# Performance work log

Hardware: AMD Instinct MI355X
Metric: run time of the kernel (lower is better)

## Reference

```python
import jax, jax.numpy as jnp
import numpy as np

DIM = 128
CODEBOOK_SIZE = 1024


def setup_inputs() -> dict:
    key = jax.random.key(0)
    kx, ke = jax.random.split(key)
    x = jax.random.normal(kx, (16, 4096, DIM), dtype=jnp.float32)
    # kaiming_uniform_ on (codebook_size, dim): bound = sqrt(6 / fan_in), fan_in = dim
    bound = float(np.sqrt(6.0 / DIM))
    embed = jax.random.uniform(ke, (CODEBOOK_SIZE, DIM), dtype=jnp.float32,
                               minval=-bound, maxval=bound)
    return {"x": x, "embed": embed}


def reference(x, embed):
    orig_shape = x.shape
    flat = x.reshape(-1, x.shape[-1])                     # [N, D]
    x2 = jnp.sum(flat * flat, axis=1, keepdims=True)      # [N, 1]
    e2 = jnp.sum(embed * embed, axis=1)                   # [K]
    dist = -(x2 - 2.0 * (flat @ embed.T) + e2[None, :])   # [N, K]
    embed_ind = jnp.argmax(dist, axis=-1)                 # [N]
    embed_ind = embed_ind.reshape(orig_shape[:-1])        # [B, S]
    quantize = jnp.take(embed, embed_ind, axis=0)         # [B, S, D]
    return quantize, embed_ind
```

## Files before the change

### kernel.cpp

```cpp
#include <hip/hip_runtime.h>

#define DIM     128
#define NCODES  1024
#define TILE_M  64
#define BSTR    272
#define FLAGThr 0.018f
#define RPB     4
#define RGRID   1024

typedef __attribute__((ext_vector_type(8))) _Float16 half8;
typedef __attribute__((ext_vector_type(4))) _Float16 half4;
typedef __attribute__((ext_vector_type(4))) float    f32x4;


__global__ __launch_bounds__(256) void setup_kernel(
    const float* __restrict__ embed, double* __restrict__ e2d,
    float* __restrict__ e2f, _Float16* __restrict__ eh,
    float* __restrict__ embedT, int* __restrict__ cnt)
{
  __shared__ float tile[64][132];
  __shared__ double psum[4][64];
  if (blockIdx.x == 0 && threadIdx.x == 0) *cnt = 0;
  const int c0 = blockIdx.x * 64;
  const int t  = threadIdx.x;

  const f32x4* E4 = (const f32x4*)(embed + (size_t)c0 * DIM);
  #pragma unroll
  for (int i = 0; i < 8; ++i) {
    int e = t + i * 256;
    int r = e >> 5, c4 = e & 31;
    f32x4 v = E4[e];
    *(f32x4*)&tile[r][c4 * 4] = v;
    half4 h;
    h[0] = (_Float16)v[0]; h[1] = (_Float16)v[1];
    h[2] = (_Float16)v[2]; h[3] = (_Float16)v[3];
    *(half4*)&eh[(size_t)(c0 + r) * DIM + c4 * 4] = h;
  }
  __syncthreads();

  {
    int r = t & 63, part = t >> 6;
    double s = 0.0;
    #pragma unroll
    for (int k = 0; k < 32; ++k) {
      float v = tile[r][part * 32 + k];
      s += (double)v * v;
    }
    psum[part][r] = s;
  }
  __syncthreads();
  if (t < 64) {
    double s = psum[0][t] + psum[1][t] + psum[2][t] + psum[3][t];
    e2d[c0 + t] = s;
    e2f[c0 + t] = (float)s;
  }

  #pragma unroll
  for (int i = 0; i < 32; ++i) {
    int idx = t + i * 256;
    int k = idx >> 6, c = idx & 63;
    embedT[(size_t)k * NCODES + c0 + c] = tile[c][k];
  }
}

__global__ __launch_bounds__(256, 2) void pass1_kernel(
    const float* __restrict__ x, const float* __restrict__ embed,
    const _Float16* __restrict__ eh, const float* __restrict__ e2f,
    float* __restrict__ outQ, float* __restrict__ outIdx,
    int* __restrict__ cnt, int* __restrict__ list)
{
  __shared__ __align__(16) unsigned char lds[256 * BSTR];
  __shared__ float rb_best[4][TILE_M];
  __shared__ float rb_sec [4][TILE_M];
  __shared__ int   fidx[TILE_M];

  const int tid  = threadIdx.x;
  const int row0 = blockIdx.x * TILE_M;
  _Float16* xh = (_Float16*)lds;

  {
    const f32x4* x4 = (const f32x4*)(x + (size_t)row0 * DIM);
    #pragma unroll
    for (int i = 0; i < 8; ++i) {
      int e = tid + i * 256;
      int r = e >> 5, c4 = e & 31;
      f32x4 v = x4[e];
      half4 h;
      h[0] = (_Float16)v[0]; h[1] = (_Float16)v[1];
      h[2] = (_Float16)v[2]; h[3] = (_Float16)v[3];
      *(half4*)&xh[r * 136 + c4 * 4] = h;
    }
  }
  __syncthreads();

  const int l  = tid & 63, w = tid >> 6;
  const int rl = l & 15,  q = l >> 4;
  const int col0 = q * 8;

  half8 afrag[4][4];
  #pragma unroll
  for (int m = 0; m < 4; ++m)
    #pragma unroll
    for (int ks = 0; ks < 4; ++ks)
      afrag[m][ks] = *(const half8*)&xh[(m * 16 + rl) * 136 + ks * 32 + col0];

  float bestp[16], secp[16];
  #pragma unroll
  for (int s = 0; s < 16; ++s) { bestp[s] = -3.0e38f; secp[s] = -3.3e38f; }

  f32x4 t0[16];
  {
    const f32x4* src = (const f32x4*)eh;
    #pragma unroll
    for (int i = 0; i < 16; ++i) t0[i] = src[tid + i * 256];
  }
  __syncthreads();

  #pragma unroll
  for (int st = 0; st < 4; ++st) {
    #pragma unroll
    for (int i = 0; i < 16; ++i) {
      int e = tid + i * 256;
      *(f32x4*)&lds[(e >> 4) * BSTR + (e & 15) * 16] = t0[i];
    }
    f32x4 t1[16];
    if (st < 3) {
      const f32x4* src = (const f32x4*)(eh + (size_t)(st + 1) * 256 * DIM);
      #pragma unroll
      for (int i = 0; i < 16; ++i) t1[i] = src[tid + i * 256];
    }
    float vinit[4];
    #pragma unroll
    for (int sub = 0; sub < 4; ++sub)
      vinit[sub] = fmaf(-0.5f, e2f[st * 256 + w * 64 + sub * 16 + rl], -16.0f);

    __syncthreads();

    #pragma unroll
    for (int sub = 0; sub < 4; ++sub) {
      const int codeL  = w * 64 + sub * 16 + rl;
      const int mycode = st * 256 + codeL;
      half8 bfrag[4];
      #pragma unroll
      for (int ks = 0; ks < 4; ++ks)
        bfrag[ks] = *(const half8*)&lds[codeL * BSTR + ks * 64 + q * 16];
      f32x4 acc[4];
      #pragma unroll
      for (int m = 0; m < 4; ++m)
        acc[m] = (f32x4){vinit[sub], vinit[sub], vinit[sub], vinit[sub]};
      #pragma unroll
      for (int ks = 0; ks < 4; ++ks)
        #pragma unroll
        for (int m = 0; m < 4; ++m)
          acc[m] = __builtin_amdgcn_mfma_f32_16x16x32_f16(afrag[m][ks], bfrag[ks], acc[m], 0, 0, 0);
      #pragma unroll
      for (int m = 0; m < 4; ++m)
        #pragma unroll
        for (int r = 0; r < 4; ++r) {
          const int s = m * 4 + r;
          float scp = __int_as_float((__float_as_int(acc[m][r]) & ~1023) | mycode);
          secp[s]  = __builtin_amdgcn_fmed3f(scp, bestp[s], secp[s]);
          bestp[s] = fmaxf(bestp[s], scp);
        }
    }
    if (st < 3) {
      __syncthreads();
      #pragma unroll
      for (int i = 0; i < 16; ++i) t0[i] = t1[i];
    }
  }

  #pragma unroll
  for (int off = 1; off < 16; off <<= 1) {
    #pragma unroll
    for (int s = 0; s < 16; ++s) {
      float ob = __shfl_xor(bestp[s], off, 16);
      float os = __shfl_xor(secp[s],  off, 16);
      secp[s]  = fmaxf(__builtin_amdgcn_fmed3f(bestp[s], ob, secp[s]), os);
      bestp[s] = fmaxf(bestp[s], ob);
    }
  }
  if (rl == 0) {
    #pragma unroll
    for (int m = 0; m < 4; ++m)
      #pragma unroll
      for (int r = 0; r < 4; ++r) {
        int s = m * 4 + r;
        int row = m * 16 + q * 4 + r;
        rb_best[w][row] = bestp[s];
        rb_sec [w][row] = secp[s];
      }
  }
  __syncthreads();

  if (tid < TILE_M) {
    float bv = rb_best[0][tid], sv = rb_sec[0][tid];
    #pragma unroll
    for (int ww = 1; ww < 4; ++ww) {
      float ob = rb_best[ww][tid], os = rb_sec[ww][tid];
      sv = fmaxf(__builtin_amdgcn_fmed3f(bv, ob, sv), os);
      bv = fmaxf(bv, ob);
    }
    int bi = __float_as_int(bv) & 1023;
    int grow = row0 + tid;
    outIdx[grow] = (float)bi;
    fidx[tid] = bi;
    if (bv - sv <= FLAGThr) {
      int p = atomicAdd(cnt, 1);
      list[p] = grow;
    }
  }
  __syncthreads();

  {
    const f32x4* E4   = (const f32x4*)embed;
    f32x4*       out4 = (f32x4*)(outQ + (size_t)row0 * DIM);
    #pragma unroll
    for (int i = 0; i < 8; ++i) {
      int e = tid + i * 256;
      int r = e >> 5, c4 = e & 31;
      out4[e] = E4[fidx[r] * 32 + c4];
    }
  }
}

__global__ __launch_bounds__(256) void refine2_kernel(
    const float* __restrict__ x, const float* __restrict__ embed,
    const float* __restrict__ embedT,
    const double* __restrict__ e2d, const float* __restrict__ e2f,
    float* __restrict__ outQ, float* __restrict__ outIdx,
    const int* __restrict__ cnt, const int* __restrict__ list)
{
  __shared__ f32x4 xst[DIM];
  __shared__ float rb1[RPB][4], rb2[RPB][4];
  __shared__ int   ri1[RPB][4], ri2[RPB][4];
  __shared__ int   cand[RPB][2];

  const int t = threadIdx.x;
  const int l = t & 63, w = t >> 6;
  const int n = *cnt;
  float* xsf = (float*)xst;

  for (int base = blockIdx.x * RPB; base < n; base += RGRID * RPB) {
    const int nr = min(RPB, n - base);
    #pragma unroll
    for (int i = 0; i < 2; ++i) {
      int idx = t + i * 256;
      int r = idx >> 7, k = idx & 127;
      float v = 0.f;
      if (r < nr) v = x[(size_t)list[base + r] * DIM + k];
      xsf[k * RPB + r] = v;
    }
    __syncthreads();

    f32x4 dot[RPB];
    #pragma unroll
    for (int r = 0; r < RPB; ++r) dot[r] = (f32x4){0.f, 0.f, 0.f, 0.f};
    const f32x4* eT4 = (const f32x4*)embedT;
    #pragma unroll 4
    for (int k = 0; k < DIM; ++k) {
      f32x4 e4  = eT4[k * 256 + t];
      f32x4 xk4 = xst[k];
      #pragma unroll
      for (int r = 0; r < RPB; ++r) {
        dot[r][0] = fmaf(xk4[r], e4[0], dot[r][0]);
        dot[r][1] = fmaf(xk4[r], e4[1], dot[r][1]);
        dot[r][2] = fmaf(xk4[r], e4[2], dot[r][2]);
        dot[r][3] = fmaf(xk4[r], e4[3], dot[r][3]);
      }
    }

    #pragma unroll
    for (int r = 0; r < RPB; ++r) {
      float b1 = 3.4e38f, b2 = 3.4e38f; int i1 = 0, i2 = 0;
      #pragma unroll
      for (int j = 0; j < 4; ++j) {
        int c = 4 * t + j;
        float sc = fmaf(-2.0f, dot[r][j], e2f[c]);
        bool better = (sc < b1);
        float lv = better ? b1 : sc;  int li = better ? i1 : c;
        if (better) { b1 = sc; i1 = c; }
        bool t2 = (lv < b2) || (lv == b2 && li < i2);
        if (t2) { b2 = lv; i2 = li; }
      }
      #pragma unroll
      for (int off = 1; off < 64; off <<= 1) {
        float o1 = __shfl_xor(b1, off, 64); int oi1 = __shfl_xor(i1, off, 64);
        float o2 = __shfl_xor(b2, off, 64); int oi2 = __shfl_xor(i2, off, 64);
        bool take = (o1 < b1) || (o1 == b1 && oi1 < i1);
        float n1 = take ? o1 : b1; int ni1 = take ? oi1 : i1;
        float lo = take ? b1 : o1; int loi = take ? i1 : oi1;
        float c2v = take ? o2 : b2; int c2i = take ? oi2 : i2;
        bool u2 = (c2v < lo) || (c2v == lo && c2i < loi);
        b1 = n1; i1 = ni1;
        b2 = u2 ? c2v : lo; i2 = u2 ? c2i : loi;
      }
      if (l == 0) { rb1[r][w] = b1; ri1[r][w] = i1; rb2[r][w] = b2; ri2[r][w] = i2; }
    }
    __syncthreads();

    if (t < RPB) {
      float v1 = rb1[t][0], v2 = rb2[t][0]; int j1 = ri1[t][0], j2 = ri2[t][0];
      #pragma unroll
      for (int ww = 1; ww < 4; ++ww) {
        float o1 = rb1[t][ww], o2 = rb2[t][ww]; int oi1 = ri1[t][ww], oi2 = ri2[t][ww];
        bool take = (o1 < v1) || (o1 == v1 && oi1 < j1);
        float n1 = take ? o1 : v1; int ni1 = take ? oi1 : j1;
        float lo = take ? v1 : o1; int loi = take ? j1 : oi1;
        float c2v = take ? o2 : v2; int c2i = take ? oi2 : j2;
        bool u2 = (c2v < lo) || (c2v == lo && c2i < loi);
        v1 = n1; j1 = ni1; v2 = u2 ? c2v : lo; j2 = u2 ? c2i : loi;
      }
      cand[t][0] = j1; cand[t][1] = j2;
    }
    __syncthreads();

    if (w < nr) {
      int c1 = cand[w][0], c2 = cand[w][1];
      float xa = xsf[l * RPB + w], xb = xsf[(l + 64) * RPB + w];
      double p1 = (double)xa * (double)embed[(size_t)c1 * DIM + l]
                + (double)xb * (double)embed[(size_t)c1 * DIM + 64 + l];
      double p2 = (double)xa * (double)embed[(size_t)c2 * DIM + l]
                + (double)xb * (double)embed[(size_t)c2 * DIM + 64 + l];
      #pragma unroll
      for (int off = 1; off < 64; off <<= 1) {
        p1 += __shfl_xor(p1, off, 64);
        p2 += __shfl_xor(p2, off, 64);
      }
      double s1 = e2d[c1] - 2.0 * p1;
      double s2 = e2d[c2] - 2.0 * p2;
      int widx = ((s2 < s1) || (s2 == s1 && c2 < c1)) ? c2 : c1;
      int row = list[base + w];
      if (l == 0) outIdx[row] = (float)widx;
      outQ[(size_t)row * DIM + l]      = embed[(size_t)widx * DIM + l];
      outQ[(size_t)row * DIM + 64 + l] = embed[(size_t)widx * DIM + 64 + l];
    }
    __syncthreads();
  }
}

extern "C" void kernel_launch(void* const* d_in, const int* in_sizes, int n_in,
                              void* d_out, int out_size, void* d_ws, size_t ws_size,
                              hipStream_t stream) {
  const float* x     = (const float*)d_in[0];
  const float* embed = (const float*)d_in[1];
  const int N = in_sizes[0] / DIM;

  float* out    = (float*)d_out;
  float* outQ   = out;
  float* outIdx = out + (size_t)N * DIM;

  char* ws = (char*)d_ws;
  double*   e2d  = (double*)  (ws);
  float*    e2f  = (float*)   (ws + 8192);
  _Float16* eh   = (_Float16*)(ws + 12288);
  float*    eT   = (float*)   (ws + 274432);
  int*      cnt  = (int*)     (ws + 798720);
  int*      list = (int*)     (ws + 798976);

  setup_kernel  <<<NCODES / 64, 256, 0, stream>>>(embed, e2d, e2f, eh, eT, cnt);
  pass1_kernel  <<<N / TILE_M,  256, 0, stream>>>(x, embed, eh, e2f, outQ, outIdx, cnt, list);
  refine2_kernel<<<RGRID,       256, 0, stream>>>(x, embed, eT, e2d, e2f, outQ, outIdx, cnt, list);
}
```

Measured before the change: 140.6 us.

## Stream codebook via global_load_lds double-buffering with XOR-swizzled LDS layout

Pass1 now copies the half-precision codebook straight from global memory into LDS using global_load_lds DMA, in 64-code chunks that are double-buffered so the next chunk loads while the current one is computed. The padded LDS stride is replaced by an XOR swizzle, pre-applied to the codebook in setup, which avoids bank conflicts and cuts LDS to 48KB so three blocks can share a CU. The refine kernel handles 8 rows per block instead of 4 on a half-size grid, reusing each loaded embedding column across more rows. The trade-off is a barrier on every one of 16 chunks instead of 4 stages, plus extra FMA registers in refine.

```diff
diff --git a/kernel.cpp b/kernel.cpp
--- a/kernel.cpp
+++ b/kernel.cpp
@@ -3,19 +3,24 @@
 #define DIM     128
 #define NCODES  1024
 #define TILE_M  64
-#define BSTR    272
 #define FLAGThr 0.018f
-#define RPB     4
-#define RGRID   1024
+#define RPB     8
+#define RGRID   512
 
 typedef __attribute__((ext_vector_type(8))) _Float16 half8;
 typedef __attribute__((ext_vector_type(4))) _Float16 half4;
 typedef __attribute__((ext_vector_type(4))) float    f32x4;
 
 
+typedef __attribute__((address_space(1))) const void gv_t;
+typedef __attribute__((address_space(3))) void       lv_t;
+__device__ __forceinline__ void dma16(const void* g, void* l) {
+  __builtin_amdgcn_global_load_lds((gv_t*)g, (lv_t*)l, 16, 0, 0);
+}
+
 __global__ __launch_bounds__(256) void setup_kernel(
     const float* __restrict__ embed, double* __restrict__ e2d,
-    float* __restrict__ e2f, _Float16* __restrict__ eh,
+    float* __restrict__ e2f, unsigned char* __restrict__ eh,
     float* __restrict__ embedT, int* __restrict__ cnt)
 {
   __shared__ float tile[64][132];
@@ -34,7 +39,8 @@
     half4 h;
     h[0] = (_Float16)v[0]; h[1] = (_Float16)v[1];
     h[2] = (_Float16)v[2]; h[3] = (_Float16)v[3];
-    *(half4*)&eh[(size_t)(c0 + r) * DIM + c4 * 4] = h;
+    int j = c4 >> 1;
+    *(half4*)(eh + (size_t)(c0 + r) * 256 + ((j ^ (r & 15)) * 16) + (c4 & 1) * 8) = h;
   }
   __syncthreads();
 
@@ -63,111 +69,105 @@
   }
 }
 
-__global__ __launch_bounds__(256, 2) void pass1_kernel(
+__global__ __launch_bounds__(256, 3) void pass1_kernel(
     const float* __restrict__ x, const float* __restrict__ embed,
-    const _Float16* __restrict__ eh, const float* __restrict__ e2f,
+    const unsigned char* __restrict__ eh, const float* __restrict__ e2f,
     float* __restrict__ outQ, float* __restrict__ outIdx,
     int* __restrict__ cnt, int* __restrict__ list)
 {
-  __shared__ __align__(16) unsigned char lds[256 * BSTR];
+  __shared__ __align__(16) unsigned char lds[49152];
   __shared__ float rb_best[4][TILE_M];
   __shared__ float rb_sec [4][TILE_M];
   __shared__ int   fidx[TILE_M];
 
   const int tid  = threadIdx.x;
   const int row0 = blockIdx.x * TILE_M;
-  _Float16* xh = (_Float16*)lds;
-
-  {
-    const f32x4* x4 = (const f32x4*)(x + (size_t)row0 * DIM);
-    #pragma unroll
-    for (int i = 0; i < 8; ++i) {
-      int e = tid + i * 256;
-      int r = e >> 5, c4 = e & 31;
-      f32x4 v = x4[e];
-      half4 h;
-      h[0] = (_Float16)v[0]; h[1] = (_Float16)v[1];
-      h[2] = (_Float16)v[2]; h[3] = (_Float16)v[3];
-      *(half4*)&xh[r * 136 + c4 * 4] = h;
-    }
-  }
-  __syncthreads();
-
   const int l  = tid & 63, w = tid >> 6;
   const int rl = l & 15,  q = l >> 4;
-  const int col0 = q * 8;
+
+  {
+    int off = (w * 4 + (tid & 63) / 64) * 0;
+    (void)off;
+    #pragma unroll
+    for (int i = 0; i < 4; ++i) {
+      int boff = (i * 4 + w) * 1024 + l * 16;
+      dma16(eh + boff, lds + 16384 + boff);
+    }
+  }
+
+  {
+    #pragma unroll
+    for (int i = 0; i < 4; ++i) {
+      int g = tid + i * 256;
+      int r = g >> 4, j = g & 15;
+      const f32x4* xs = (const f32x4*)(x + (size_t)(row0 + r) * DIM + j * 8);
+      f32x4 v0 = xs[0], v1 = xs[1];
+      half8 h;
+      h[0] = (_Float16)v0[0]; h[1] = (_Float16)v0[1];
+      h[2] = (_Float16)v0[2]; h[3] = (_Float16)v0[3];
+      h[4] = (_Float16)v1[0]; h[5] = (_Float16)v1[1];
+      h[6] = (_Float16)v1[2]; h[7] = (_Float16)v1[3];
+      *(half8*)(lds + r * 256 + (j ^ (r & 15)) * 16) = h;
+    }
+  }
+  __syncthreads();
 
   half8 afrag[4][4];
   #pragma unroll
   for (int m = 0; m < 4; ++m)
     #pragma unroll
     for (int ks = 0; ks < 4; ++ks)
-      afrag[m][ks] = *(const half8*)&xh[(m * 16 + rl) * 136 + ks * 32 + col0];
+      afrag[m][ks] = *(const half8*)(lds + (m * 16 + rl) * 256 + ((ks * 4 + q) ^ rl) * 16);
 
   float bestp[16], secp[16];
   #pragma unroll
   for (int s = 0; s < 16; ++s) { bestp[s] = -3.0e38f; secp[s] = -3.3e38f; }
 
-  f32x4 t0[16];
-  {
-    const f32x4* src = (const f32x4*)eh;
-    #pragma unroll
-    for (int i = 0; i < 16; ++i) t0[i] = src[tid + i * 256];
-  }
-  __syncthreads();
-
-  #pragma unroll
-  for (int st = 0; st < 4; ++st) {
-    #pragma unroll
-    for (int i = 0; i < 16; ++i) {
-      int e = tid + i * 256;
-      *(f32x4*)&lds[(e >> 4) * BSTR + (e & 15) * 16] = t0[i];
-    }
-    f32x4 t1[16];
-    if (st < 3) {
-      const f32x4* src = (const f32x4*)(eh + (size_t)(st + 1) * 256 * DIM);
-      #pragma unroll
-      for (int i = 0; i < 16; ++i) t1[i] = src[tid + i * 256];
-    }
-    float vinit[4];
-    #pragma unroll
-    for (int sub = 0; sub < 4; ++sub)
-      vinit[sub] = fmaf(-0.5f, e2f[st * 256 + w * 64 + sub * 16 + rl], -16.0f);
-
-    __syncthreads();
-
-    #pragma unroll
-    for (int sub = 0; sub < 4; ++sub) {
-      const int codeL  = w * 64 + sub * 16 + rl;
-      const int mycode = st * 256 + codeL;
-      half8 bfrag[4];
-      #pragma unroll
-      for (int ks = 0; ks < 4; ++ks)
-        bfrag[ks] = *(const half8*)&lds[codeL * BSTR + ks * 64 + q * 16];
-      f32x4 acc[4];
+  float e2cur = e2f[w * 16 + rl];
+
+  #pragma unroll 2
+  for (int ch = 0; ch < 16; ++ch) {
+    unsigned char* bufC = lds + 16384 + (ch & 1) * 16384;
+    if (ch < 15) {
+      unsigned char* bufN = lds + 16384 + ((ch + 1) & 1) * 16384;
+      const unsigned char* src = eh + (size_t)(ch + 1) * 16384;
+      #pragma unroll
+      for (int i = 0; i < 4; ++i) {
+        int boff = (i * 4 + w) * 1024 + l * 16;
+        dma16(src + boff, bufN + boff);
+      }
+    }
+    float e2nxt = (ch < 15) ? e2f[(ch + 1) * 64 + w * 16 + rl] : 0.f;
+
+    const int codeG = ch * 64 + w * 16 + rl;
+    const float vinit = fmaf(-0.5f, e2cur, -16.0f);
+
+    half8 bfrag[4];
+    #pragma unroll
+    for (int ks = 0; ks < 4; ++ks)
+      bfrag[ks] = *(const half8*)(bufC + (w * 16 + rl) * 256 + ((ks * 4 + q) ^ rl) * 16);
+
+    f32x4 acc[4];
+    #pragma unroll
+    for (int m = 0; m < 4; ++m) acc[m] = (f32x4){vinit, vinit, vinit, vinit};
+    #pragma unroll
+    for (int ks = 0; ks < 4; ++ks)
       #pragma unroll
       for (int m = 0; m < 4; ++m)
-        acc[m] = (f32x4){vinit[sub], vinit[sub], vinit[sub], vinit[sub]};
-      #pragma unroll
-      for (int ks = 0; ks < 4; ++ks)
-        #pragma unroll
-        for (int m = 0; m < 4; ++m)
-          acc[m] = __builtin_amdgcn_mfma_f32_16x16x32_f16(afrag[m][ks], bfrag[ks], acc[m], 0, 0, 0);
-      #pragma unroll
-      for (int m = 0; m < 4; ++m)
-        #pragma unroll
-        for (int r = 0; r < 4; ++r) {
-          const int s = m * 4 + r;
-          float scp = __int_as_float((__float_as_int(acc[m][r]) & ~1023) | mycode);
-          secp[s]  = __builtin_amdgcn_fmed3f(scp, bestp[s], secp[s]);
-          bestp[s] = fmaxf(bestp[s], scp);
-        }
-    }
-    if (st < 3) {
-      __syncthreads();
-      #pragma unroll
-      for (int i = 0; i < 16; ++i) t0[i] = t1[i];
-    }
+        acc[m] = __builtin_amdgcn_mfma_f32_16x16x32_f16(afrag[m][ks], bfrag[ks], acc[m], 0, 0, 0);
+
+    #pragma unroll
+    for (int m = 0; m < 4; ++m)
+      #pragma unroll
+      for (int r = 0; r < 4; ++r) {
+        const int s = m * 4 + r;
+        float scp = __int_as_float((__float_as_int(acc[m][r]) & ~1023) | codeG);
+        secp[s]  = __builtin_amdgcn_fmed3f(scp, bestp[s], secp[s]);
+        bestp[s] = fmaxf(bestp[s], scp);
+      }
+
+    e2cur = e2nxt;
+    __syncthreads();
   }
 
   #pragma unroll
@@ -231,7 +231,7 @@
     float* __restrict__ outQ, float* __restrict__ outIdx,
     const int* __restrict__ cnt, const int* __restrict__ list)
 {
-  __shared__ f32x4 xst[DIM];
+  __shared__ float xsf[DIM * RPB];
   __shared__ float rb1[RPB][4], rb2[RPB][4];
   __shared__ int   ri1[RPB][4], ri2[RPB][4];
   __shared__ int   cand[RPB][2];
@@ -239,12 +239,11 @@
   const int t = threadIdx.x;
   const int l = t & 63, w = t >> 6;
   const int n = *cnt;
-  float* xsf = (float*)xst;
 
   for (int base = blockIdx.x * RPB; base < n; base += RGRID * RPB) {
     const int nr = min(RPB, n - base);
     #pragma unroll
-    for (int i = 0; i < 2; ++i) {
+    for (int i = 0; i < 4; ++i) {
       int idx = t + i * 256;
       int r = idx >> 7, k = idx & 127;
       float v = 0.f;
@@ -259,14 +258,19 @@
     const f32x4* eT4 = (const f32x4*)embedT;
     #pragma unroll 4
     for (int k = 0; k < DIM; ++k) {
-      f32x4 e4  = eT4[k * 256 + t];
-      f32x4 xk4 = xst[k];
-      #pragma unroll
-      for (int r = 0; r < RPB; ++r) {
-        dot[r][0] = fmaf(xk4[r], e4[0], dot[r][0]);
-        dot[r][1] = fmaf(xk4[r], e4[1], dot[r][1]);
-        dot[r][2] = fmaf(xk4[r], e4[2], dot[r][2]);
-        dot[r][3] = fmaf(xk4[r], e4[3], dot[r][3]);
+      f32x4 e4 = eT4[k * 256 + t];
+      f32x4 xa = *(const f32x4*)&xsf[k * RPB];
+      f32x4 xb = *(const f32x4*)&xsf[k * RPB + 4];
+      #pragma unroll
+      for (int r = 0; r < 4; ++r) {
+        dot[r][0] = fmaf(xa[r], e4[0], dot[r][0]);
+        dot[r][1] = fmaf(xa[r], e4[1], dot[r][1]);
+        dot[r][2] = fmaf(xa[r], e4[2], dot[r][2]);
+        dot[r][3] = fmaf(xa[r], e4[3], dot[r][3]);
+        dot[r+4][0] = fmaf(xb[r], e4[0], dot[r+4][0]);
+        dot[r+4][1] = fmaf(xb[r], e4[1], dot[r+4][1]);
+        dot[r+4][2] = fmaf(xb[r], e4[2], dot[r+4][2]);
+        dot[r+4][3] = fmaf(xb[r], e4[3], dot[r+4][3]);
       }
     }
 
@@ -315,9 +319,9 @@
     }
     __syncthreads();
 
-    if (w < nr) {
-      int c1 = cand[w][0], c2 = cand[w][1];
-      float xa = xsf[l * RPB + w], xb = xsf[(l + 64) * RPB + w];
+    for (int rr = w; rr < nr; rr += 4) {
+      int c1 = cand[rr][0], c2 = cand[rr][1];
+      float xa = xsf[l * RPB + rr], xb = xsf[(l + 64) * RPB + rr];
       double p1 = (double)xa * (double)embed[(size_t)c1 * DIM + l]
                 + (double)xb * (double)embed[(size_t)c1 * DIM + 64 + l];
       double p2 = (double)xa * (double)embed[(size_t)c2 * DIM + l]
@@ -330,7 +334,7 @@
       double s1 = e2d[c1] - 2.0 * p1;
       double s2 = e2d[c2] - 2.0 * p2;
       int widx = ((s2 < s1) || (s2 == s1 && c2 < c1)) ? c2 : c1;
-      int row = list[base + w];
+      int row = list[base + rr];
       if (l == 0) outIdx[row] = (float)widx;
       outQ[(size_t)row * DIM + l]      = embed[(size_t)widx * DIM + l];
       outQ[(size_t)row * DIM + 64 + l] = embed[(size_t)widx * DIM + 64 + l];
@@ -351,12 +355,12 @@
   float* outIdx = out + (size_t)N * DIM;
 
   char* ws = (char*)d_ws;
-  double*   e2d  = (double*)  (ws);
-  float*    e2f  = (float*)   (ws + 8192);
-  _Float16* eh   = (_Float16*)(ws + 12288);
-  float*    eT   = (float*)   (ws + 274432);
-  int*      cnt  = (int*)     (ws + 798720);
-  int*      list = (int*)     (ws + 798976);
+  double*        e2d  = (double*)       (ws);
+  float*         e2f  = (float*)        (ws + 8192);
+  unsigned char* eh   = (unsigned char*)(ws + 12288);
+  float*         eT   = (float*)        (ws + 274432);
+  int*           cnt  = (int*)          (ws + 798720);
+  int*           list = (int*)          (ws + 798976);
 
   setup_kernel  <<<NCODES / 64, 256, 0, stream>>>(embed, e2d, e2f, eh, eT, cnt);
   pass1_kernel  <<<N / TILE_M,  256, 0, stream>>>(x, embed, eh, e2f, outQ, outIdx, cnt, list);
```

Measured after the change: 149.5 us. +6.3%, slower.
